# Kernel optimization log

Hardware: AMD Instinct MI355X
Metric: run time of the kernel (lower is better)

The kernel has to match this reference:

```python
import jax, jax.numpy as jnp
import numpy as np
import math

B, LQ, LK = 4, 512, 512
D_MODEL, NHEAD, NLABELS = 512, 8, 8
D_Q = D_MODEL // NHEAD


def setup_inputs() -> dict:
    key = jax.random.key(0)
    ks = jax.random.split(key, 12)
    xavier = lambda k, shape: jax.random.uniform(
        k, shape, jnp.float32,
        -math.sqrt(6.0 / (shape[0] + shape[1])), math.sqrt(6.0 / (shape[0] + shape[1])))
    return {
        "q": jax.random.normal(ks[0], (B, LQ, D_MODEL), jnp.float32),
        "k": jax.random.normal(ks[1], (B, LK, D_MODEL), jnp.float32),
        "edge_mask": jax.random.randint(ks[2], (B, LQ, LK, NLABELS), 0, 2).astype(jnp.float32),
        "padding_mask": jax.random.randint(ks[3], (B, LQ, LK), 0, 2).astype(jnp.float32),
        "w_q_w": xavier(ks[4], (D_MODEL, D_MODEL)),
        "w_q_b": jnp.zeros((D_MODEL,), jnp.float32),
        "w_k": xavier(ks[5], (D_MODEL, D_MODEL)),
        "w_v": xavier(ks[6], (D_MODEL, D_MODEL)),
        "w_h_w": xavier(ks[7], (D_MODEL, D_MODEL)),
        "w_h_b": jnp.zeros((D_MODEL,), jnp.float32),
        "b_ks": xavier(ks[8], (NLABELS, D_Q)),
        "b_vs": xavier(ks[9], (NLABELS, D_Q)),
    }


def reference(q, k, edge_mask, padding_mask, w_q_w, w_q_b, w_k, w_v, w_h_w, w_h_b, b_ks, b_vs):
    sz_b, len_q, _ = q.shape
    len_k = k.shape[1]
    temp = np.power(D_Q, 0.5).astype(np.float32)

    # projections -> (nhead, B, L, d_q), matching torch permute(2,0,1,3)
    query = (q @ w_q_w.T + w_q_b).reshape(sz_b, len_q, NHEAD, D_Q).transpose(2, 0, 1, 3)
    key = (k @ w_k.T).reshape(sz_b, len_k, NHEAD, D_Q).transpose(2, 0, 1, 3)
    value = (k @ w_v.T).reshape(sz_b, len_k, NHEAD, D_Q).transpose(2, 0, 1, 3)

    # content scores + relation-bias scores
    qk = jnp.einsum('hbqd,hbkd->hbqk', query, key)
    key_rel = jnp.einsum('bqkl,ld->bqkd', edge_mask, b_ks)      # (B,Lq,Lk,d_q)
    qkr = jnp.einsum('hbqd,bqkd->hbqk', query, key_rel)
    output_attention_weights = (qk + qkr) / temp                # pre-mask, as returned by torch

    # mask where no edge label AND padding_mask==1
    relation_mask = (edge_mask.sum(-1) + (1.0 - padding_mask)) == 0  # (B,Lq,Lk)
    rm = relation_mask[None, :, :, :]                                # broadcast over heads
    attn = jnp.where(rm, -jnp.inf, output_attention_weights)
    attn = jax.nn.softmax(attn, axis=-1)
    attn = jnp.where(rm, 0.0, attn)

    # value aggregation: content + relation values
    qv = jnp.einsum('hbqk,hbkd->hbqd', attn, value)
    val_rel = jnp.einsum('bqkl,ld->bqkd', edge_mask, b_vs)
    qvr = jnp.einsum('hbqk,bqkd->hbqd', attn, val_rel)

    out = (qv + qvr).transpose(1, 2, 0, 3).reshape(sz_b, len_q, D_MODEL)
    out = out @ w_h_w.T + w_h_b
    return out, output_attention_weights.reshape(NHEAD * sz_b, len_q, len_k)
```

## Files before the change

### kernel.cpp

```cpp
#include <hip/hip_runtime.h>
#include <math.h>

#define NB 4
#define LQ 512
#define LK 512
#define DM 512
#define NH 8
#define DQ 64
#define NL 8
#define QT 32
#define PSTR 520

typedef short bf16x8 __attribute__((ext_vector_type(8)));
typedef float f32x4 __attribute__((ext_vector_type(4)));

__device__ __forceinline__ unsigned short f2bf(float x) {
    unsigned u = __float_as_uint(x);
    u += 0x7fff + ((u >> 16) & 1);
    return (unsigned short)(u >> 16);
}
__device__ __forceinline__ float bf2f(unsigned x) {
    return __uint_as_float(x << 16);
}
__device__ __forceinline__ uint4 pack8(float4 a, float4 b) {
    uint4 o;
    o.x = (unsigned)f2bf(a.x) | ((unsigned)f2bf(a.y) << 16);
    o.y = (unsigned)f2bf(a.z) | ((unsigned)f2bf(a.w) << 16);
    o.z = (unsigned)f2bf(b.x) | ((unsigned)f2bf(b.y) << 16);
    o.w = (unsigned)f2bf(b.z) | ((unsigned)f2bf(b.w) << 16);
    return o;
}
__device__ __forceinline__ void gld16(const void* g, void* l) {
    __builtin_amdgcn_global_load_lds(
        (const __attribute__((address_space(1))) void*)g,
        (__attribute__((address_space(3))) void*)l, 16, 0, 0);
}

__global__ __launch_bounds__(256) void empack_kernel(const float* __restrict__ em,
                                                     const float* __restrict__ pad,
                                                     unsigned short* __restrict__ Pk) {
    const int bq = blockIdx.x;
    const int k0 = threadIdx.x * 2;
    const float4* e4 = (const float4*)(em + (size_t)bq * (LK * NL) + (size_t)k0 * NL);
    const float4 v0 = e4[0], v1 = e4[1], v2 = e4[2], v3 = e4[3];
    const float2 pv = *(const float2*)(pad + (size_t)bq * LK + k0);
    unsigned b0 = 0, b1 = 0;
    b0 |= (v0.x != 0.f) << 0; b0 |= (v0.y != 0.f) << 1;
    b0 |= (v0.z != 0.f) << 2; b0 |= (v0.w != 0.f) << 3;
    b0 |= (v1.x != 0.f) << 4; b0 |= (v1.y != 0.f) << 5;
    b0 |= (v1.z != 0.f) << 6; b0 |= (v1.w != 0.f) << 7;
    b0 |= (pv.x != 0.f) << 8;
    b1 |= (v2.x != 0.f) << 0; b1 |= (v2.y != 0.f) << 1;
    b1 |= (v2.z != 0.f) << 2; b1 |= (v2.w != 0.f) << 3;
    b1 |= (v3.x != 0.f) << 4; b1 |= (v3.y != 0.f) << 5;
    b1 |= (v3.z != 0.f) << 6; b1 |= (v3.w != 0.f) << 7;
    b1 |= (pv.y != 0.f) << 8;
    *(unsigned*)(Pk + (size_t)bq * LK + k0) = b0 | (b1 << 16);
}

__global__ __launch_bounds__(256) void proj_all(const float* __restrict__ qg,
                                                const float* __restrict__ kg,
                                                const float* __restrict__ wq,
                                                const float* __restrict__ wk,
                                                const float* __restrict__ wv,
                                                const float* __restrict__ w_q_b,
                                                unsigned short* __restrict__ Qp,
                                                unsigned short* __restrict__ Kp,
                                                unsigned short* __restrict__ Vt) {
    __shared__ __align__(16) short As[64 * 32];
    __shared__ __align__(16) short Bs[64 * 32];
    const float* A; const float* W; const float* bias; unsigned short* C; int mode;
    switch (blockIdx.z) {
        case 0:  A = qg; W = wq; bias = w_q_b;  C = Qp; mode = 0; break;
        case 1:  A = kg; W = wk; bias = nullptr; C = Kp; mode = 0; break;
        default: A = kg; W = wv; bias = nullptr; C = Vt; mode = 1; break;
    }
    const int tid = threadIdx.x, wave = tid >> 6, lane = tid & 63;
    const int quad = lane >> 4, l16 = lane & 15;
    const int wr = wave >> 1, wc = wave & 1;
    const int m0 = blockIdx.x * 64, n0 = blockIdx.y * 64;
    const int srow = tid >> 2, scol = (tid & 3) * 8;
    const float* Ab = A + (size_t)(m0 + srow) * DM + scol;
    const float* Wb = W + (size_t)(n0 + srow) * DM + scol;

    f32x4 acc[2][2];
    const f32x4 zz = {0.f, 0.f, 0.f, 0.f};
#pragma unroll
    for (int i = 0; i < 2; ++i)
#pragma unroll
        for (int j = 0; j < 2; ++j) acc[i][j] = zz;

    for (int k0 = 0; k0 < DM; k0 += 32) {
        const float4 a0 = *(const float4*)(Ab + k0);
        const float4 a1 = *(const float4*)(Ab + k0 + 4);
        const float4 b0 = *(const float4*)(Wb + k0);
        const float4 b1 = *(const float4*)(Wb + k0 + 4);
        __syncthreads();
        *(uint4*)&As[srow * 32 + scol] = pack8(a0, a1);
        *(uint4*)&Bs[srow * 32 + scol] = pack8(b0, b1);
        __syncthreads();
        bf16x8 af[2], bf[2];
#pragma unroll
        for (int i = 0; i < 2; ++i)
            af[i] = *(const bf16x8*)&As[(wr * 32 + i * 16 + l16) * 32 + quad * 8];
#pragma unroll
        for (int j = 0; j < 2; ++j)
            bf[j] = *(const bf16x8*)&Bs[(wc * 32 + j * 16 + l16) * 32 + quad * 8];
#pragma unroll
        for (int i = 0; i < 2; ++i)
#pragma unroll
            for (int j = 0; j < 2; ++j)
                acc[i][j] = __builtin_amdgcn_mfma_f32_16x16x32_bf16(af[i], bf[j], acc[i][j], 0, 0, 0);
    }
#pragma unroll
    for (int i = 0; i < 2; ++i)
#pragma unroll
        for (int r = 0; r < 4; ++r) {
            const int gm = m0 + wr * 32 + i * 16 + quad * 4 + r;
#pragma unroll
            for (int j = 0; j < 2; ++j) {
                const int gn = n0 + wc * 32 + j * 16 + l16;
                float v = acc[i][j][r];
                if (bias) v += bias[gn];
                if (mode == 0) C[(size_t)gm * DM + gn] = f2bf(v);
                else C[(size_t)(gm >> 9) * (DM * LK) + (size_t)gn * LK + (gm & 511)] = f2bf(v);
            }
        }
}

__global__ __launch_bounds__(512, 4) void attn_fused(
        const unsigned short* __restrict__ Qp,
        const unsigned short* __restrict__ Kp,
        const unsigned short* __restrict__ Vt,
        const unsigned short* __restrict__ Pk,
        const float* __restrict__ b_ks,
        const float* __restrict__ b_vs,
        float* __restrict__ weights,
        unsigned short* __restrict__ Hb) {
    __shared__ __align__(16) short Qs[QT * 64];
    __shared__ __align__(16) short Kc[128 * 64];
    __shared__ __align__(16) short Ps[QT * PSTR];
    __shared__ float svS[QT * NL];
    __shared__ float tS[QT * NL];
    __shared__ float redA[QT * 8];
    __shared__ float redB[QT * 8];

    const int tid = threadIdx.x, wave = tid >> 6, lane = tid & 63;
    const int quad = lane >> 4, l16 = lane & 15;
    const int q0 = blockIdx.x * QT;
    const int z = blockIdx.y, h = z >> 2, b = z & 3;

    if (tid < 256) {
        const int row = tid >> 3, off = (tid & 7) * 8;
        gld16(Qp + (size_t)(b * LQ + q0 + row) * DM + h * DQ + off,
              (char*)Qs + wave * 1024);
    }

    f32x4 acc[4][2];
    const f32x4 zz = {0.f, 0.f, 0.f, 0.f};
#pragma unroll
    for (int c = 0; c < 4; ++c) { acc[c][0] = zz; acc[c][1] = zz; }

    for (int c = 0; c < 4; ++c) {
#pragma unroll
        for (int it = 0; it < 2; ++it) {
            const int e = it * 512 + tid;
            const int kr = c * 128 + (e >> 3), off = (e & 7) * 8;
            gld16(Kp + (size_t)(b * LK + kr) * DM + h * DQ + off,
                  (char*)Kc + it * 8192 + wave * 1024);
        }
        __syncthreads();
#pragma unroll
        for (int kd = 0; kd < 64; kd += 32) {
            const bf16x8 bfv = *(const bf16x8*)&Kc[(wave * 16 + l16) * 64 + kd + quad * 8];
#pragma unroll
            for (int i = 0; i < 2; ++i) {
                const bf16x8 afv = *(const bf16x8*)&Qs[(i * 16 + l16) * 64 + kd + quad * 8];
                acc[c][i] = __builtin_amdgcn_mfma_f32_16x16x32_bf16(afv, bfv, acc[c][i], 0, 0, 0);
            }
        }
        if (c == 0 && tid < 256) {
            const int row = tid >> 3, l = tid & 7;
            float s = 0.f;
#pragma unroll
            for (int d = 0; d < DQ; ++d)
                s = fmaf(bf2f((unsigned short)Qs[row * 64 + d]), b_ks[l * DQ + d], s);
            svS[row * 8 + l] = s;
        }
        __syncthreads();
    }

#pragma unroll
    for (int it = 0; it < 2; ++it) {
        const int e = it * 512 + tid;
        const int dd = e >> 4, off = (e & 15) * 8;
        gld16(Vt + (size_t)(b * DM + h * DQ + dd) * LK + off,
              (char*)Kc + it * 8192 + wave * 1024);
    }

#pragma unroll
    for (int i = 0; i < 2; ++i)
#pragma unroll
        for (int r = 0; r < 4; ++r) {
            const int row = i * 16 + quad * 4 + r;
            const int gq = q0 + row;
            const f32x4 sv0 = *(const f32x4*)&svS[row * 8];
            const f32x4 sv1 = *(const f32x4*)&svS[row * 8 + 4];
            const unsigned short* prow = Pk + (size_t)(b * LQ + gq) * LK;
            float* wrow = weights + ((size_t)z * LQ + gq) * LK;
            float pm = -__builtin_inff();
#pragma unroll
            for (int c = 0; c < 4; ++c) {
                const int col = c * 128 + wave * 16 + l16;
                const unsigned w_ = prow[col];
                float rel = 0.f;
                rel = fmaf((float)((w_ >> 0) & 1), sv0[0], rel);
                rel = fmaf((float)((w_ >> 1) & 1), sv0[1], rel);
                rel = fmaf((float)((w_ >> 2) & 1), sv0[2], rel);
                rel = fmaf((float)((w_ >> 3) & 1), sv0[3], rel);
                rel = fmaf((float)((w_ >> 4) & 1), sv1[0], rel);
                rel = fmaf((float)((w_ >> 5) & 1), sv1[1], rel);
                rel = fmaf((float)((w_ >> 6) & 1), sv1[2], rel);
                rel = fmaf((float)((w_ >> 7) & 1), sv1[3], rel);
                const float wv = (acc[c][i][r] + rel) * 0.125f;
                wrow[col] = wv;
                const float m = ((w_ & 0x1FFu) == 0x100u) ? -__builtin_inff() : wv;
                acc[c][i][r] = m;
                pm = fmaxf(pm, m);
            }
#pragma unroll
            for (int o = 1; o < 16; o <<= 1) pm = fmaxf(pm, __shfl_xor(pm, o, 64));
            if (l16 == 0) redA[row * 8 + wave] = pm;
        }
    __syncthreads();

#pragma unroll
    for (int i = 0; i < 2; ++i)
#pragma unroll
        for (int r = 0; r < 4; ++r) {
            const int row = i * 16 + quad * 4 + r;
            const f32x4 ra = *(const f32x4*)&redA[row * 8];
            const f32x4 rb = *(const f32x4*)&redA[row * 8 + 4];
            const float rmax = fmaxf(fmaxf(fmaxf(ra[0], ra[1]), fmaxf(ra[2], ra[3])),
                                     fmaxf(fmaxf(rb[0], rb[1]), fmaxf(rb[2], rb[3])));
            float psum = 0.f;
#pragma unroll
            for (int c = 0; c < 4; ++c) {
                const float e = __expf(acc[c][i][r] - rmax);
                acc[c][i][r] = e;
                psum += e;
            }
#pragma unroll
            for (int o = 1; o < 16; o <<= 1) psum += __shfl_xor(psum, o, 64);
            if (l16 == 0) redB[row * 8 + wave] = psum;
        }
    __syncthreads();

#pragma unroll
    for (int i = 0; i < 2; ++i)
#pragma unroll
        for (int r = 0; r < 4; ++r) {
            const int row = i * 16 + quad * 4 + r;
            const f32x4 sa = *(const f32x4*)&redB[row * 8];
            const f32x4 sb = *(const f32x4*)&redB[row * 8 + 4];
            const float tot = ((sa[0] + sa[1]) + (sa[2] + sa[3])) +
                              ((sb[0] + sb[1]) + (sb[2] + sb[3]));
            const float inv = 1.0f / tot;
#pragma unroll
            for (int c = 0; c < 4; ++c) {
                const int col = c * 128 + wave * 16 + l16;
                Ps[row * PSTR + col] = (short)f2bf(acc[c][i][r] * inv);
            }
        }
    __syncthreads();

    {
        const int row = tid >> 4, l = (tid >> 1) & 7, half = tid & 1;
        const unsigned* pw = (const unsigned*)(Pk + (size_t)(b * LQ + q0 + row) * LK + half * 256);
        const unsigned* aw = (const unsigned*)&Ps[row * PSTR + half * 256];
        float tv = 0.f;
#pragma unroll 4
        for (int kk = 0; kk < 128; ++kk) {
            const unsigned wbits = pw[kk];
            const unsigned av = aw[kk];
            tv = fmaf((float)((wbits >> l) & 1),        bf2f(av & 0xffffu), tv);
            tv = fmaf((float)((wbits >> (16 + l)) & 1), bf2f(av >> 16), tv);
        }
        tv += __shfl_xor(tv, 1, 64);
        if (half == 0) tS[row * 8 + l] = tv;
    }

    f32x4 oacc = zz;
    const int mi = wave & 1, ni = wave >> 1;
    for (int vc = 0; vc < 4; ++vc) {
        if (vc > 0) {
            __syncthreads();
#pragma unroll
            for (int it = 0; it < 2; ++it) {
                const int e = it * 512 + tid;
                const int dd = e >> 4, off = (e & 15) * 8;
                gld16(Vt + (size_t)(b * DM + h * DQ + dd) * LK + vc * 128 + off,
                      (char*)Kc + it * 8192 + wave * 1024);
            }
        }
        __syncthreads();
#pragma unroll
        for (int kd = 0; kd < 128; kd += 32) {
            const bf16x8 afv = *(const bf16x8*)&Ps[(mi * 16 + l16) * PSTR + vc * 128 + kd + quad * 8];
            const bf16x8 bfv = *(const bf16x8*)&Kc[(ni * 16 + l16) * 128 + kd + quad * 8];
            oacc = __builtin_amdgcn_mfma_f32_16x16x32_bf16(afv, bfv, oacc, 0, 0, 0);
        }
    }

    const int gd = ni * 16 + l16;
    float bvv[NL];
#pragma unroll
    for (int l = 0; l < NL; ++l) bvv[l] = b_vs[l * DQ + gd];
#pragma unroll
    for (int r = 0; r < 4; ++r) {
        const int row = mi * 16 + quad * 4 + r;
        const float* tp = &tS[row * 8];
        float o = oacc[r];
#pragma unroll
        for (int l = 0; l < NL; ++l) o = fmaf(tp[l], bvv[l], o);
        Hb[(size_t)(b * LQ + q0 + row) * DM + h * DQ + gd] = f2bf(o);
    }
}

__global__ __launch_bounds__(256) void outproj_mfma(const unsigned short* __restrict__ Hb,
                                                    const float* __restrict__ W,
                                                    const float* __restrict__ bias,
                                                    float* __restrict__ C) {
    __shared__ __align__(16) short As[64 * 32];
    __shared__ __align__(16) short Bs[64 * 32];
    const int tid = threadIdx.x, wave = tid >> 6, lane = tid & 63;
    const int quad = lane >> 4, l16 = lane & 15;
    const int wr = wave >> 1, wc = wave & 1;
    const int m0 = blockIdx.x * 64, n0 = blockIdx.y * 64;
    const int srow = tid >> 2, scol = (tid & 3) * 8;
    const unsigned short* Ag = Hb + (size_t)m0 * DM;
    const float* Wb = W + (size_t)(n0 + srow) * DM + scol;

    f32x4 acc[2][2];
    const f32x4 zz = {0.f, 0.f, 0.f, 0.f};
#pragma unroll
    for (int i = 0; i < 2; ++i)
#pragma unroll
        for (int j = 0; j < 2; ++j) acc[i][j] = zz;

    for (int k0 = 0; k0 < DM; k0 += 32) {
        const float4 b0 = *(const float4*)(Wb + k0);
        const float4 b1 = *(const float4*)(Wb + k0 + 4);
        __syncthreads();
        gld16(Ag + (size_t)(tid >> 2) * DM + k0 + (tid & 3) * 8,
              (char*)As + wave * 1024);
        *(uint4*)&Bs[srow * 32 + scol] = pack8(b0, b1);
        __syncthreads();
        bf16x8 af[2], bf[2];
#pragma unroll
        for (int i = 0; i < 2; ++i)
            af[i] = *(const bf16x8*)&As[(wr * 32 + i * 16 + l16) * 32 + quad * 8];
#pragma unroll
        for (int j = 0; j < 2; ++j)
            bf[j] = *(const bf16x8*)&Bs[(wc * 32 + j * 16 + l16) * 32 + quad * 8];
#pragma unroll
        for (int i = 0; i < 2; ++i)
#pragma unroll
            for (int j = 0; j < 2; ++j)
                acc[i][j] = __builtin_amdgcn_mfma_f32_16x16x32_bf16(af[i], bf[j], acc[i][j], 0, 0, 0);
    }
#pragma unroll
    for (int i = 0; i < 2; ++i)
#pragma unroll
        for (int r = 0; r < 4; ++r) {
            const int gm = m0 + wr * 32 + i * 16 + quad * 4 + r;
#pragma unroll
            for (int j = 0; j < 2; ++j) {
                const int gn = n0 + wc * 32 + j * 16 + l16;
                C[(size_t)gm * DM + gn] = acc[i][j][r] + bias[gn];
            }
        }
}

extern "C" void kernel_launch(void* const* d_in, const int* in_sizes, int n_in,
                              void* d_out, int out_size, void* d_ws, size_t ws_size,
                              hipStream_t stream) {
    const float* q     = (const float*)d_in[0];
    const float* k     = (const float*)d_in[1];
    const float* em    = (const float*)d_in[2];
    const float* pad   = (const float*)d_in[3];
    const float* w_q_w = (const float*)d_in[4];
    const float* w_q_b = (const float*)d_in[5];
    const float* w_k   = (const float*)d_in[6];
    const float* w_v   = (const float*)d_in[7];
    const float* w_h_w = (const float*)d_in[8];
    const float* w_h_b = (const float*)d_in[9];
    const float* b_ks  = (const float*)d_in[10];
    const float* b_vs  = (const float*)d_in[11];

    float* out     = (float*)d_out;
    float* weights = out + (size_t)NB * LQ * DM;

    char* ws = (char*)d_ws;
    unsigned short* Qp = (unsigned short*)(ws + 0);
    unsigned short* Kp = (unsigned short*)(ws + 2097152);
    unsigned short* Vt = (unsigned short*)(ws + 4194304);
    unsigned short* Hb = (unsigned short*)(ws + 6291456);
    unsigned short* Pk = (unsigned short*)(ws + 8388608);

    empack_kernel<<<dim3(NB * LQ), 256, 0, stream>>>(em, pad, Pk);
    proj_all<<<dim3(32, 8, 3), 256, 0, stream>>>(q, k, w_q_w, w_k, w_v, w_q_b, Qp, Kp, Vt);
    attn_fused<<<dim3(LQ / QT, 32), 512, 0, stream>>>(Qp, Kp, Vt, Pk, b_ks, b_vs, weights, Hb);
    outproj_mfma<<<dim3(32, 8), 256, 0, stream>>>(Hb, w_h_w, w_h_b, out);
}
```

Measured before the change: 176.0 us.

## Pre-convert inputs to bf16, merge softmax reductions, vectorize relation-weight loop

```diff
diff --git a/kernel.cpp b/kernel.cpp
--- a/kernel.cpp
+++ b/kernel.cpp
@@ -22,96 +22,130 @@
 __device__ __forceinline__ float bf2f(unsigned x) {
     return __uint_as_float(x << 16);
 }
-__device__ __forceinline__ uint4 pack8(float4 a, float4 b) {
-    uint4 o;
-    o.x = (unsigned)f2bf(a.x) | ((unsigned)f2bf(a.y) << 16);
-    o.y = (unsigned)f2bf(a.z) | ((unsigned)f2bf(a.w) << 16);
-    o.z = (unsigned)f2bf(b.x) | ((unsigned)f2bf(b.y) << 16);
-    o.w = (unsigned)f2bf(b.z) | ((unsigned)f2bf(b.w) << 16);
-    return o;
-}
 __device__ __forceinline__ void gld16(const void* g, void* l) {
     __builtin_amdgcn_global_load_lds(
         (const __attribute__((address_space(1))) void*)g,
         (__attribute__((address_space(3))) void*)l, 16, 0, 0);
 }
 
-__global__ __launch_bounds__(256) void empack_kernel(const float* __restrict__ em,
-                                                     const float* __restrict__ pad,
-                                                     unsigned short* __restrict__ Pk) {
-    const int bq = blockIdx.x;
-    const int k0 = threadIdx.x * 2;
-    const float4* e4 = (const float4*)(em + (size_t)bq * (LK * NL) + (size_t)k0 * NL);
-    const float4 v0 = e4[0], v1 = e4[1], v2 = e4[2], v3 = e4[3];
-    const float2 pv = *(const float2*)(pad + (size_t)bq * LK + k0);
-    unsigned b0 = 0, b1 = 0;
-    b0 |= (v0.x != 0.f) << 0; b0 |= (v0.y != 0.f) << 1;
-    b0 |= (v0.z != 0.f) << 2; b0 |= (v0.w != 0.f) << 3;
-    b0 |= (v1.x != 0.f) << 4; b0 |= (v1.y != 0.f) << 5;
-    b0 |= (v1.z != 0.f) << 6; b0 |= (v1.w != 0.f) << 7;
-    b0 |= (pv.x != 0.f) << 8;
-    b1 |= (v2.x != 0.f) << 0; b1 |= (v2.y != 0.f) << 1;
-    b1 |= (v2.z != 0.f) << 2; b1 |= (v2.w != 0.f) << 3;
-    b1 |= (v3.x != 0.f) << 4; b1 |= (v3.y != 0.f) << 5;
-    b1 |= (v3.z != 0.f) << 6; b1 |= (v3.w != 0.f) << 7;
-    b1 |= (pv.y != 0.f) << 8;
-    *(unsigned*)(Pk + (size_t)bq * LK + k0) = b0 | (b1 << 16);
-}
-
-__global__ __launch_bounds__(256) void proj_all(const float* __restrict__ qg,
-                                                const float* __restrict__ kg,
-                                                const float* __restrict__ wq,
-                                                const float* __restrict__ wk,
-                                                const float* __restrict__ wv,
+__global__ __launch_bounds__(256) void prep_kernel(
+        const float* __restrict__ q,  const float* __restrict__ k,
+        const float* __restrict__ wq, const float* __restrict__ wk,
+        const float* __restrict__ wv, const float* __restrict__ wh,
+        const float* __restrict__ em, const float* __restrict__ pad,
+        unsigned short* __restrict__ qb,  unsigned short* __restrict__ kb,
+        unsigned short* __restrict__ wqb, unsigned short* __restrict__ wkb,
+        unsigned short* __restrict__ wvb, unsigned short* __restrict__ whb,
+        unsigned short* __restrict__ Pk) {
+    const int tid = threadIdx.x;
+    const int y = blockIdx.y;
+    if (y < 6) {
+        const float* s; unsigned short* d; int n;
+        switch (y) {
+            case 0: s = q;  d = qb;  n = NB * LQ * DM; break;
+            case 1: s = k;  d = kb;  n = NB * LK * DM; break;
+            case 2: s = wq; d = wqb; n = DM * DM; break;
+            case 3: s = wk; d = wkb; n = DM * DM; break;
+            case 4: s = wv; d = wvb; n = DM * DM; break;
+            default: s = wh; d = whb; n = DM * DM; break;
+        }
+        const int i = blockIdx.x * 256 + tid;
+        if (i * 8 >= n) return;
+        const float4* sv = (const float4*)s;
+        const float4 a = sv[2 * (size_t)i], b = sv[2 * (size_t)i + 1];
+        uint4 o;
+        o.x = (unsigned)f2bf(a.x) | ((unsigned)f2bf(a.y) << 16);
+        o.y = (unsigned)f2bf(a.z) | ((unsigned)f2bf(a.w) << 16);
+        o.z = (unsigned)f2bf(b.x) | ((unsigned)f2bf(b.y) << 16);
+        o.w = (unsigned)f2bf(b.z) | ((unsigned)f2bf(b.w) << 16);
+        *(uint4*)(d + (size_t)i * 8) = o;
+    } else {
+        if (blockIdx.x >= 512) return;
+        const int row = blockIdx.x * 4 + (tid >> 6);
+        const int k0 = (tid & 63) * 8;
+        const float* eb = em + ((size_t)row * LK + k0) * NL;
+        const float4 pv0 = *(const float4*)(pad + (size_t)row * LK + k0);
+        const float4 pv1 = *(const float4*)(pad + (size_t)row * LK + k0 + 4);
+        const float pv[8] = {pv0.x, pv0.y, pv0.z, pv0.w, pv1.x, pv1.y, pv1.z, pv1.w};
+        unsigned short outv[8];
+#pragma unroll
+        for (int kk = 0; kk < 8; ++kk) {
+            const float4 v0 = *(const float4*)(eb + kk * 8);
+            const float4 v1 = *(const float4*)(eb + kk * 8 + 4);
+            unsigned b_ = 0;
+            b_ |= (v0.x != 0.f) << 0; b_ |= (v0.y != 0.f) << 1;
+            b_ |= (v0.z != 0.f) << 2; b_ |= (v0.w != 0.f) << 3;
+            b_ |= (v1.x != 0.f) << 4; b_ |= (v1.y != 0.f) << 5;
+            b_ |= (v1.z != 0.f) << 6; b_ |= (v1.w != 0.f) << 7;
+            b_ |= (pv[kk] != 0.f) << 8;
+            outv[kk] = (unsigned short)b_;
+        }
+        uint4 o;
+        o.x = (unsigned)outv[0] | ((unsigned)outv[1] << 16);
+        o.y = (unsigned)outv[2] | ((unsigned)outv[3] << 16);
+        o.z = (unsigned)outv[4] | ((unsigned)outv[5] << 16);
+        o.w = (unsigned)outv[6] | ((unsigned)outv[7] << 16);
+        *(uint4*)(Pk + (size_t)row * LK + k0) = o;
+    }
+}
+
+__device__ __forceinline__ void gemm64core(const unsigned short* __restrict__ Ag, int lda,
+                                           const unsigned short* __restrict__ Bg, int ldb,
+                                           int K, short* As, short* Bs,
+                                           f32x4 (&acc)[2][2]) {
+    const int tid = threadIdx.x;
+    const int wave = tid >> 6, lane = tid & 63;
+    const int quad = lane >> 4, l16 = lane & 15;
+    const int wr = wave >> 1, wc = wave & 1;
+    for (int k0 = 0; k0 < K; k0 += 32) {
+        __syncthreads();
+        gld16(Ag + (size_t)(tid >> 2) * lda + k0 + (tid & 3) * 8, (char*)As + wave * 1024);
+        gld16(Bg + (size_t)(tid >> 2) * ldb + k0 + (tid & 3) * 8, (char*)Bs + wave * 1024);
+        __syncthreads();
+        bf16x8 af[2], bf[2];
+#pragma unroll
+        for (int i = 0; i < 2; ++i)
+            af[i] = *(const bf16x8*)&As[(wr * 32 + i * 16 + l16) * 32 + quad * 8];
+#pragma unroll
+        for (int j = 0; j < 2; ++j)
+            bf[j] = *(const bf16x8*)&Bs[(wc * 32 + j * 16 + l16) * 32 + quad * 8];
+#pragma unroll
+        for (int i = 0; i < 2; ++i)
+#pragma unroll
+            for (int j = 0; j < 2; ++j)
+                acc[i][j] = __builtin_amdgcn_mfma_f32_16x16x32_bf16(af[i], bf[j], acc[i][j], 0, 0, 0);
+    }
+}
+
+__global__ __launch_bounds__(256) void proj_all(const unsigned short* __restrict__ qb,
+                                                const unsigned short* __restrict__ kb,
+                                                const unsigned short* __restrict__ wqb,
+                                                const unsigned short* __restrict__ wkb,
+                                                const unsigned short* __restrict__ wvb,
                                                 const float* __restrict__ w_q_b,
                                                 unsigned short* __restrict__ Qp,
                                                 unsigned short* __restrict__ Kp,
                                                 unsigned short* __restrict__ Vt) {
     __shared__ __align__(16) short As[64 * 32];
     __shared__ __align__(16) short Bs[64 * 32];
-    const float* A; const float* W; const float* bias; unsigned short* C; int mode;
+    const unsigned short* A; const unsigned short* W; const float* bias;
+    unsigned short* C; int mode;
     switch (blockIdx.z) {
-        case 0:  A = qg; W = wq; bias = w_q_b;  C = Qp; mode = 0; break;
-        case 1:  A = kg; W = wk; bias = nullptr; C = Kp; mode = 0; break;
-        default: A = kg; W = wv; bias = nullptr; C = Vt; mode = 1; break;
-    }
+        case 0:  A = qb; W = wqb; bias = w_q_b;  C = Qp; mode = 0; break;
+        case 1:  A = kb; W = wkb; bias = nullptr; C = Kp; mode = 0; break;
+        default: A = kb; W = wvb; bias = nullptr; C = Vt; mode = 1; break;
+    }
+    f32x4 acc[2][2];
+    const f32x4 zz = {0.f, 0.f, 0.f, 0.f};
+#pragma unroll
+    for (int i = 0; i < 2; ++i)
+#pragma unroll
+        for (int j = 0; j < 2; ++j) acc[i][j] = zz;
+    const int m0 = blockIdx.x * 64, n0 = blockIdx.y * 64;
+    gemm64core(A + (size_t)m0 * DM, DM, W + (size_t)n0 * DM, DM, DM, As, Bs, acc);
     const int tid = threadIdx.x, wave = tid >> 6, lane = tid & 63;
     const int quad = lane >> 4, l16 = lane & 15;
     const int wr = wave >> 1, wc = wave & 1;
-    const int m0 = blockIdx.x * 64, n0 = blockIdx.y * 64;
-    const int srow = tid >> 2, scol = (tid & 3) * 8;
-    const float* Ab = A + (size_t)(m0 + srow) * DM + scol;
-    const float* Wb = W + (size_t)(n0 + srow) * DM + scol;
-
-    f32x4 acc[2][2];
-    const f32x4 zz = {0.f, 0.f, 0.f, 0.f};
-#pragma unroll
-    for (int i = 0; i < 2; ++i)
-#pragma unroll
-        for (int j = 0; j < 2; ++j) acc[i][j] = zz;
-
-    for (int k0 = 0; k0 < DM; k0 += 32) {
-        const float4 a0 = *(const float4*)(Ab + k0);
-        const float4 a1 = *(const float4*)(Ab + k0 + 4);
-        const float4 b0 = *(const float4*)(Wb + k0);
-        const float4 b1 = *(const float4*)(Wb + k0 + 4);
-        __syncthreads();
-        *(uint4*)&As[srow * 32 + scol] = pack8(a0, a1);
-        *(uint4*)&Bs[srow * 32 + scol] = pack8(b0, b1);
-        __syncthreads();
-        bf16x8 af[2], bf[2];
-#pragma unroll
-        for (int i = 0; i < 2; ++i)
-            af[i] = *(const bf16x8*)&As[(wr * 32 + i * 16 + l16) * 32 + quad * 8];
-#pragma unroll
-        for (int j = 0; j < 2; ++j)
-            bf[j] = *(const bf16x8*)&Bs[(wc * 32 + j * 16 + l16) * 32 + quad * 8];
-#pragma unroll
-        for (int i = 0; i < 2; ++i)
-#pragma unroll
-            for (int j = 0; j < 2; ++j)
-                acc[i][j] = __builtin_amdgcn_mfma_f32_16x16x32_bf16(af[i], bf[j], acc[i][j], 0, 0, 0);
-    }
 #pragma unroll
     for (int i = 0; i < 2; ++i)
 #pragma unroll
@@ -230,7 +264,16 @@
             }
 #pragma unroll
             for (int o = 1; o < 16; o <<= 1) pm = fmaxf(pm, __shfl_xor(pm, o, 64));
-            if (l16 == 0) redA[row * 8 + wave] = pm;
+            float ps = 0.f;
+#pragma unroll
+            for (int c = 0; c < 4; ++c) {
+                const float e = __expf(acc[c][i][r] - pm);
+                acc[c][i][r] = e;
+                ps += e;
+            }
+#pragma unroll
+            for (int o = 1; o < 16; o <<= 1) ps += __shfl_xor(ps, o, 64);
+            if (l16 == 0) { redA[row * 8 + wave] = pm; redB[row * 8 + wave] = ps; }
         }
     __syncthreads();
 
@@ -239,52 +282,42 @@
 #pragma unroll
         for (int r = 0; r < 4; ++r) {
             const int row = i * 16 + quad * 4 + r;
-            const f32x4 ra = *(const f32x4*)&redA[row * 8];
-            const f32x4 rb = *(const f32x4*)&redA[row * 8 + 4];
-            const float rmax = fmaxf(fmaxf(fmaxf(ra[0], ra[1]), fmaxf(ra[2], ra[3])),
-                                     fmaxf(fmaxf(rb[0], rb[1]), fmaxf(rb[2], rb[3])));
-            float psum = 0.f;
-#pragma unroll
-            for (int c = 0; c < 4; ++c) {
-                const float e = __expf(acc[c][i][r] - rmax);
-                acc[c][i][r] = e;
-                psum += e;
-            }
-#pragma unroll
-            for (int o = 1; o < 16; o <<= 1) psum += __shfl_xor(psum, o, 64);
-            if (l16 == 0) redB[row * 8 + wave] = psum;
-        }
-    __syncthreads();
-
-#pragma unroll
-    for (int i = 0; i < 2; ++i)
-#pragma unroll
-        for (int r = 0; r < 4; ++r) {
-            const int row = i * 16 + quad * 4 + r;
+            const f32x4 pa = *(const f32x4*)&redA[row * 8];
+            const f32x4 pb = *(const f32x4*)&redA[row * 8 + 4];
             const f32x4 sa = *(const f32x4*)&redB[row * 8];
             const f32x4 sb = *(const f32x4*)&redB[row * 8 + 4];
-            const float tot = ((sa[0] + sa[1]) + (sa[2] + sa[3])) +
-                              ((sb[0] + sb[1]) + (sb[2] + sb[3]));
-            const float inv = 1.0f / tot;
+            const float M = fmaxf(fmaxf(fmaxf(pa[0], pa[1]), fmaxf(pa[2], pa[3])),
+                                  fmaxf(fmaxf(pb[0], pb[1]), fmaxf(pb[2], pb[3])));
+            const float S = sa[0] * __expf(pa[0] - M) + sa[1] * __expf(pa[1] - M)
+                          + sa[2] * __expf(pa[2] - M) + sa[3] * __expf(pa[3] - M)
+                          + sb[0] * __expf(pb[0] - M) + sb[1] * __expf(pb[1] - M)
+                          + sb[2] * __expf(pb[2] - M) + sb[3] * __expf(pb[3] - M);
+            const float own = redA[row * 8 + wave];
+            const float alpha = __expf(own - M) / S;
 #pragma unroll
             for (int c = 0; c < 4; ++c) {
                 const int col = c * 128 + wave * 16 + l16;
-                Ps[row * PSTR + col] = (short)f2bf(acc[c][i][r] * inv);
+                Ps[row * PSTR + col] = (short)f2bf(acc[c][i][r] * alpha);
             }
         }
     __syncthreads();
 
     {
         const int row = tid >> 4, l = (tid >> 1) & 7, half = tid & 1;
-        const unsigned* pw = (const unsigned*)(Pk + (size_t)(b * LQ + q0 + row) * LK + half * 256);
-        const unsigned* aw = (const unsigned*)&Ps[row * PSTR + half * 256];
+        const uint4* pw = (const uint4*)(Pk + (size_t)(b * LQ + q0 + row) * LK + half * 256);
+        const uint4* aw = (const uint4*)&Ps[row * PSTR + half * 256];
         float tv = 0.f;
 #pragma unroll 4
-        for (int kk = 0; kk < 128; ++kk) {
-            const unsigned wbits = pw[kk];
-            const unsigned av = aw[kk];
-            tv = fmaf((float)((wbits >> l) & 1),        bf2f(av & 0xffffu), tv);
-            tv = fmaf((float)((wbits >> (16 + l)) & 1), bf2f(av >> 16), tv);
+        for (int kk = 0; kk < 32; ++kk) {
+            const uint4 wb = pw[kk];
+            const uint4 av = aw[kk];
+            const unsigned w4[4] = {wb.x, wb.y, wb.z, wb.w};
+            const unsigned a4[4] = {av.x, av.y, av.z, av.w};
+#pragma unroll
+            for (int u = 0; u < 4; ++u) {
+                tv += ((w4[u] >> l) & 1)        ? bf2f(a4[u] & 0xffffu) : 0.f;
+                tv += ((w4[u] >> (16 + l)) & 1) ? bf2f(a4[u] >> 16)     : 0.f;
+            }
         }
         tv += __shfl_xor(tv, 1, 64);
         if (half == 0) tS[row * 8 + l] = tv;
@@ -302,8 +335,8 @@
                 gld16(Vt + (size_t)(b * DM + h * DQ + dd) * LK + vc * 128 + off,
                       (char*)Kc + it * 8192 + wave * 1024);
             }
-        }
-        __syncthreads();
+            __syncthreads();
+        }
 #pragma unroll
         for (int kd = 0; kd < 128; kd += 32) {
             const bf16x8 afv = *(const bf16x8*)&Ps[(mi * 16 + l16) * PSTR + vc * 128 + kd + quad * 8];
@@ -328,47 +361,22 @@
 }
 
 __global__ __launch_bounds__(256) void outproj_mfma(const unsigned short* __restrict__ Hb,
-                                                    const float* __restrict__ W,
+                                                    const unsigned short* __restrict__ whb,
                                                     const float* __restrict__ bias,
                                                     float* __restrict__ C) {
     __shared__ __align__(16) short As[64 * 32];
     __shared__ __align__(16) short Bs[64 * 32];
+    f32x4 acc[2][2];
+    const f32x4 zz = {0.f, 0.f, 0.f, 0.f};
+#pragma unroll
+    for (int i = 0; i < 2; ++i)
+#pragma unroll
+        for (int j = 0; j < 2; ++j) acc[i][j] = zz;
+    const int m0 = blockIdx.x * 64, n0 = blockIdx.y * 64;
+    gemm64core(Hb + (size_t)m0 * DM, DM, whb + (size_t)n0 * DM, DM, DM, As, Bs, acc);
     const int tid = threadIdx.x, wave = tid >> 6, lane = tid & 63;
     const int quad = lane >> 4, l16 = lane & 15;
     const int wr = wave >> 1, wc = wave & 1;
-    const int m0 = blockIdx.x * 64, n0 = blockIdx.y * 64;
-    const int srow = tid >> 2, scol = (tid & 3) * 8;
-    const unsigned short* Ag = Hb + (size_t)m0 * DM;
-    const float* Wb = W + (size_t)(n0 + srow) * DM + scol;
-
-    f32x4 acc[2][2];
-    const f32x4 zz = {0.f, 0.f, 0.f, 0.f};
-#pragma unroll
-    for (int i = 0; i < 2; ++i)
-#pragma unroll
-        for (int j = 0; j < 2; ++j) acc[i][j] = zz;
-
-    for (int k0 = 0; k0 < DM; k0 += 32) {
-        const float4 b0 = *(const float4*)(Wb + k0);
-        const float4 b1 = *(const float4*)(Wb + k0 + 4);
-        __syncthreads();
-        gld16(Ag + (size_t)(tid >> 2) * DM + k0 + (tid & 3) * 8,
-              (char*)As + wave * 1024);
-        *(uint4*)&Bs[srow * 32 + scol] = pack8(b0, b1);
-        __syncthreads();
-        bf16x8 af[2], bf[2];
-#pragma unroll
-        for (int i = 0; i < 2; ++i)
-            af[i] = *(const bf16x8*)&As[(wr * 32 + i * 16 + l16) * 32 + quad * 8];
-#pragma unroll
-        for (int j = 0; j < 2; ++j)
-            bf[j] = *(const bf16x8*)&Bs[(wc * 32 + j * 16 + l16) * 32 + quad * 8];
-#pragma unroll
-        for (int i = 0; i < 2; ++i)
-#pragma unroll
-            for (int j = 0; j < 2; ++j)
-                acc[i][j] = __builtin_amdgcn_mfma_f32_16x16x32_bf16(af[i], bf[j], acc[i][j], 0, 0, 0);
-    }
 #pragma unroll
     for (int i = 0; i < 2; ++i)
 #pragma unroll
@@ -402,14 +410,21 @@
     float* weights = out + (size_t)NB * LQ * DM;
 
     char* ws = (char*)d_ws;
-    unsigned short* Qp = (unsigned short*)(ws + 0);
-    unsigned short* Kp = (unsigned short*)(ws + 2097152);
-    unsigned short* Vt = (unsigned short*)(ws + 4194304);
-    unsigned short* Hb = (unsigned short*)(ws + 6291456);
-    unsigned short* Pk = (unsigned short*)(ws + 8388608);
-
-    empack_kernel<<<dim3(NB * LQ), 256, 0, stream>>>(em, pad, Pk);
-    proj_all<<<dim3(32, 8, 3), 256, 0, stream>>>(q, k, w_q_w, w_k, w_v, w_q_b, Qp, Kp, Vt);
+    unsigned short* qb  = (unsigned short*)(ws + 0);
+    unsigned short* kb  = (unsigned short*)(ws + 2097152);
+    unsigned short* wqb = (unsigned short*)(ws + 4194304);
+    unsigned short* wkb = (unsigned short*)(ws + 4718592);
+    unsigned short* wvb = (unsigned short*)(ws + 5242880);
+    unsigned short* whb = (unsigned short*)(ws + 5767168);
+    unsigned short* Qp  = (unsigned short*)(ws + 6291456);
+    unsigned short* Kp  = (unsigned short*)(ws + 8388608);
+    unsigned short* Vt  = (unsigned short*)(ws + 10485760);
+    unsigned short* Hb  = (unsigned short*)(ws + 12582912);
+    unsigned short* Pk  = (unsigned short*)(ws + 14680064);
+
+    prep_kernel<<<dim3(1024, 7), 256, 0, stream>>>(q, k, w_q_w, w_k, w_v, w_h_w,
+                                                   em, pad, qb, kb, wqb, wkb, wvb, whb, Pk);
+    proj_all<<<dim3(32, 8, 3), 256, 0, stream>>>(qb, kb, wqb, wkb, wvb, w_q_b, Qp, Kp, Vt);
     attn_fused<<<dim3(LQ / QT, 32), 512, 0, stream>>>(Qp, Kp, Vt, Pk, b_ks, b_vs, weights, Hb);
-    outproj_mfma<<<dim3(32, 8), 256, 0, stream>>>(Hb, w_h_w, w_h_b, out);
-}
+    outproj_mfma<<<dim3(32, 8), 256, 0, stream>>>(Hb, whb, w_h_b, out);
+}
```

Measured after the change: 174.2 us. About the same (-1.1%).
